# Optimization experiments

Hardware: AMD Instinct MI355X
Metric: run time of the kernel (lower is better)

The kernel has to match this reference:

```python
import jax, jax.numpy as jnp
import numpy as np

TOKENS, HIDDEN, N_EXPERTS = 16384, 2048, 64
JITTER_EPS = 0.01
Z_LOSS_COEFF = 0.001


def setup_inputs() -> dict:
    key = jax.random.key(0)
    k1, k2 = jax.random.split(key)
    x = jax.random.normal(k1, (TOKENS, HIDDEN), dtype=jnp.float32)
    w = jax.random.normal(k2, (N_EXPERTS, HIDDEN), dtype=jnp.float32) * 0.02  # router weight [E,H]
    return {"x": x, "w": w}


def _route_pass(scores_sel, scores, jitter_eps):
    # scores_sel: logits possibly with -inf at already-selected expert (top-2 pass)
    # scores:     original logits (used for abs/clamp factor, as in torch code)
    mx = jnp.max(scores_sel, axis=-1, keepdims=True)                      # [N,1]
    factor = jnp.maximum(jnp.abs(scores), mx)                             # scores.abs().clamp(min=mx)
    mask = jax.lax.stop_gradient((mx - scores) / factor > 2.0 * jitter_eps)
    masked_logits = jnp.where(mask, -jnp.inf, scores_sel)
    # eval path (training=False): selected_experts = argmax of (masked-for-selection) scores
    sel = jnp.argmax(scores_sel, axis=-1)[..., None]                      # [N,1] int
    gates = jax.nn.softmax(masked_logits, axis=-1)
    # mask_for_one: selected == argmax(gates) holds deterministically in eval -> 1.0
    mult = jnp.take_along_axis(gates, sel, axis=-1)                       # [N,1]
    return mult, sel


def reference(x, w):
    logits = x @ w.T                                                      # [N,E]
    # z-loss (identity on logits in forward; scalar returned for completeness)
    z_loss = Z_LOSS_COEFF * jnp.mean(jnp.square(jax.nn.logsumexp(logits, axis=-1)))
    original_gates = jax.nn.softmax(logits, axis=-1)
    # top-1 pass
    m1, s1 = _route_pass(logits, logits, JITTER_EPS)
    # top-2 pass: mask out the first selection
    e_idx = jnp.arange(logits.shape[-1])[None, :]
    scores2 = jnp.where(e_idx == s1, -jnp.inf, logits)
    m2, s2 = _route_pass(scores2, logits, JITTER_EPS)
    multiplier = jnp.concatenate([m1, m2], axis=-1)                       # [N,2]
    selected_experts = jnp.concatenate([s1, s2], axis=-1)                 # [N,2]
    return multiplier, original_gates, selected_experts, z_loss
```

## Files before the change

### kernel.cpp

```cpp
#include <hip/hip_runtime.h>
#include <math.h>

#define TOKENS 16384
#define HIDDEN 2048
#define NEXP   64
#define MT     16
#define NBLK   (TOKENS / MT)
#define BK     256
#define NCH    (HIDDEN / BK)
#define ROWB   1024

#define GATES_OFF (TOKENS * 2)
#define SEL_OFF   (GATES_OFF + TOKENS * NEXP)
#define Z_OFF     (SEL_OFF + TOKENS * 2)

#define WIMG_BYTES (NEXP * HIDDEN * 2 * 2)

typedef __attribute__((ext_vector_type(8))) _Float16 f16x8;
typedef __attribute__((ext_vector_type(4))) float    f32x4;

__device__ __forceinline__ float wave_sum64(float v) {
    #pragma unroll
    for (int s = 1; s < 64; s <<= 1) v += __shfl_xor(v, s, 64);
    return v;
}

__device__ __forceinline__ void dma16(const void* g, void* l) {
    __builtin_amdgcn_global_load_lds(
        (const __attribute__((address_space(1))) unsigned int*)g,
        (__attribute__((address_space(3))) unsigned int*)l, 16, 0, 0);
}

__global__ __launch_bounds__(256) void wconvert(
    const float* __restrict__ w, uint4* __restrict__ wimg)
{
    const int s = blockIdx.x * 256 + threadIdx.x;
    const int c    = s >> 10;
    const int r    = s & 1023;
    const int l    = r & 63;
    const int nt   = (r >> 6) & 1;
    const int kh   = (r >> 7) & 1;
    const int term = (r >> 8) & 1;
    const int eh   = (r >> 9) & 1;
    const int e = eh * 32 + nt * 16 + (l & 15);
    const int k = c * 64 + kh * 32 + (l >> 4) * 8;

    const float* src = w + (size_t)e * HIDDEN + k;
    union { _Float16 f[8]; uint4 u; } o;
    #pragma unroll
    for (int j = 0; j < 8; ++j) {
        const float v = src[j];
        const _Float16 h = (_Float16)v;
        o.f[j] = (term == 0) ? h : (_Float16)((v - (float)h) * 4096.f);
    }
    wimg[s] = o.u;
}

__device__ __forceinline__ void cvt_split(const float4 a, const float4 b,
                                          f16x8& hi, f16x8& lo) {
    union { _Float16 f[8]; f16x8 v; } H, L;
    #pragma unroll
    for (int j = 0; j < 4; ++j) {
        const float s0 = (&a.x)[j];
        const float s1 = (&b.x)[j];
        const _Float16 h0 = (_Float16)s0;
        const _Float16 h1 = (_Float16)s1;
        H.f[j]     = h0;
        H.f[j + 4] = h1;
        L.f[j]     = (_Float16)((s0 - (float)h0) * 4096.f);
        L.f[j + 4] = (_Float16)((s1 - (float)h1) * 4096.f);
    }
    hi = H.v; lo = L.v;
}

__global__ __launch_bounds__(256, 3) void router_main(
    const float* __restrict__ x, const uint4* __restrict__ wimg,
    float* __restrict__ out, float* __restrict__ zpartial)
{
    __shared__ __align__(16) unsigned char smem[2 * MT * ROWB];
    __shared__ float zred[4];
    float* lg = (float*)smem;

    const int tid  = threadIdx.x;
    const int wv   = __builtin_amdgcn_readfirstlane(tid >> 6);
    const int lane = tid & 63;
    const int t0   = blockIdx.x * MT;

    const int row_r = lane & 15;
    const int kgrp  = lane >> 4;
    const int sr    = (row_r & 7) << 4;

    const float* xg[4];
    #pragma unroll
    for (int p = 0; p < 4; ++p) {
        const int row  = wv * 4 + p;
        const int srow = (row & 7) << 4;
        xg[p] = x + (size_t)(t0 + row) * HIDDEN + (((lane * 16) ^ srow) >> 2);
    }

    f32x4 acc0[4], acc1[4];
    #pragma unroll
    for (int g = 0; g < 4; ++g) { acc0[g] = (f32x4)0.f; acc1[g] = (f32x4)0.f; }

    #pragma unroll
    for (int p = 0; p < 4; ++p)
        dma16(xg[p], smem + (wv * 4 + p) * ROWB);
    __syncthreads();

    #pragma unroll
    for (int c = 0; c < NCH; ++c) {
        const int buf = c & 1;

        const uint4* p0 = wimg + (size_t)(c * 4 + wv) * 1024 + lane;
        f16x8 bh[2][4], bl[2][4];
        #pragma unroll
        for (int st = 0; st < 2; ++st) {
            const uint4* p = p0 + st * 128;
            bh[st][0] = *(const f16x8*)(p);
            bh[st][1] = *(const f16x8*)(p + 64);
            bh[st][2] = *(const f16x8*)(p + 512);
            bh[st][3] = *(const f16x8*)(p + 576);
            bl[st][0] = *(const f16x8*)(p + 256);
            bl[st][1] = *(const f16x8*)(p + 320);
            bl[st][2] = *(const f16x8*)(p + 768);
            bl[st][3] = *(const f16x8*)(p + 832);
        }

        if (c + 1 < NCH) {
            #pragma unroll
            for (int p = 0; p < 4; ++p)
                dma16(xg[p] + (c + 1) * BK,
                      smem + (buf ^ 1) * (MT * ROWB) + (wv * 4 + p) * ROWB);
        }

        const unsigned char* abase = smem + buf * (MT * ROWB) + row_r * ROWB;
        #pragma unroll
        for (int st = 0; st < 2; ++st) {
            const int kb0 = wv * 256 + st * 128 + kgrp * 32;
            const float4 va = *(const float4*)(abase + (kb0 ^ sr));
            const float4 vb = *(const float4*)(abase + ((kb0 + 16) ^ sr));
            f16x8 Ah, Al;
            cvt_split(va, vb, Ah, Al);
            #pragma unroll
            for (int g = 0; g < 4; ++g) {
                acc0[g] = __builtin_amdgcn_mfma_f32_16x16x32_f16(Ah, bh[st][g], acc0[g], 0, 0, 0);
                acc1[g] = __builtin_amdgcn_mfma_f32_16x16x32_f16(Ah, bl[st][g], acc1[g], 0, 0, 0);
                acc1[g] = __builtin_amdgcn_mfma_f32_16x16x32_f16(Al, bh[st][g], acc1[g], 0, 0, 0);
            }
        }

        __syncthreads();
    }

    #pragma unroll
    for (int g = 0; g < 4; ++g)
        #pragma unroll
        for (int r = 0; r < 4; ++r) {
            const int tok = kgrp * 4 + r;
            const int e   = (g >> 1) * 32 + (g & 1) * 16 + row_r;
            lg[wv * (MT * 66) + tok * 66 + e] = acc0[g][r] + acc1[g][r] * (1.f / 4096.f);
        }
    __syncthreads();

    float zsum = 0.f;
    for (int tt = 0; tt < 4; ++tt) {
        const int t = wv * 4 + tt;
        const int li = t * 66 + lane;
        const float v = lg[0 * (MT * 66) + li] + lg[1 * (MT * 66) + li]
                      + lg[2 * (MT * 66) + li] + lg[3 * (MT * 66) + li];

        float bv = v; int bi = lane;
        #pragma unroll
        for (int s = 1; s < 64; s <<= 1) {
            const float ov = __shfl_xor(bv, s, 64);
            const int   oi = __shfl_xor(bi, s, 64);
            if (ov > bv || (ov == bv && oi < bi)) { bv = ov; bi = oi; }
        }
        const float max1 = bv; const int s1 = bi;

        const float e1 = expf(v - max1);
        const float sume = wave_sum64(e1);
        out[GATES_OFF + (size_t)(t0 + t) * NEXP + lane] = e1 / sume;
        const float lse = max1 + logf(sume);
        zsum += lse * lse;

        const bool mask1 = (max1 - v) > 0.02f * fmaxf(fabsf(v), max1);
        const float sum1 = wave_sum64(mask1 ? 0.f : e1);

        float bv2 = (lane == s1) ? -INFINITY : v; int bi2 = lane;
        #pragma unroll
        for (int s = 1; s < 64; s <<= 1) {
            const float ov = __shfl_xor(bv2, s, 64);
            const int   oi = __shfl_xor(bi2, s, 64);
            if (ov > bv2 || (ov == bv2 && oi < bi2)) { bv2 = ov; bi2 = oi; }
        }
        const float max2 = bv2; const int s2 = bi2;

        const bool mask2 = (max2 - v) > 0.02f * fmaxf(fabsf(v), max2);
        const float p2v = (mask2 || lane == s1) ? 0.f : expf(v - max2);
        const float sum2 = wave_sum64(p2v);

        if (lane == 0) {
            const size_t trow = (size_t)(t0 + t) * 2;
            out[trow + 0] = 1.f / sum1;
            out[trow + 1] = 1.f / sum2;
            out[SEL_OFF + trow + 0] = (float)s1;
            out[SEL_OFF + trow + 1] = (float)s2;
        }
    }

    if (lane == 0) zred[wv] = zsum;
    __syncthreads();
    if (tid == 0)
        zpartial[blockIdx.x] = zred[0] + zred[1] + zred[2] + zred[3];
}

__global__ __launch_bounds__(256) void zfinal(
    const float* __restrict__ zpartial, float* __restrict__ out)
{
    const int tid = threadIdx.x;
    float v = zpartial[tid] + zpartial[tid + 256]
            + zpartial[tid + 512] + zpartial[tid + 768];
    v = wave_sum64(v);
    __shared__ float red[4];
    if ((tid & 63) == 0) red[tid >> 6] = v;
    __syncthreads();
    if (tid == 0) {
        const float tot = red[0] + red[1] + red[2] + red[3];
        out[Z_OFF] = 0.001f * (tot / (float)TOKENS);
    }
}

extern "C" void kernel_launch(void* const* d_in, const int* in_sizes, int n_in,
                              void* d_out, int out_size, void* d_ws, size_t ws_size,
                              hipStream_t stream) {
    const float* x = (const float*)d_in[0];
    const float* w = (const float*)d_in[1];
    float* out = (float*)d_out;

    uint4* wimg     = (uint4*)d_ws;
    float* zpartial = (float*)((char*)d_ws + WIMG_BYTES);

    wconvert<<<128, 256, 0, stream>>>(w, wimg);
    router_main<<<NBLK, 256, 0, stream>>>(x, wimg, out, zpartial);
    zfinal<<<1, 256, 0, stream>>>(zpartial, out);
}
```

Measured before the change: 213.6 us.

## Use single-wave blocks covering full K, dropping cross-wave reduction and barriers

Each 16-token block now runs as one 64-lane wave that walks the whole hidden dimension instead of splitting K across four waves. This removes the LDS partial-logit reduction and all block barriers, and the routing softmax/top-2 epilogue works directly from the MFMA accumulators with 16-lane shuffles. The trade-off is four times as much serial MFMA and weight-load work per wave, with the x tile DMA double-buffered per wave and guarded only by vmcnt waits. Occupancy now relies on many small blocks instead of large ones.

```diff
diff --git a/kernel.cpp b/kernel.cpp
--- a/kernel.cpp
+++ b/kernel.cpp
@@ -8,7 +8,7 @@
 #define NBLK   (TOKENS / MT)
 #define BK     256
 #define NCH    (HIDDEN / BK)
-#define ROWB   1024
+#define CB     16384
 
 #define GATES_OFF (TOKENS * 2)
 #define SEL_OFF   (GATES_OFF + TOKENS * NEXP)
@@ -73,146 +73,146 @@
     hi = H.v; lo = L.v;
 }
 
-__global__ __launch_bounds__(256, 3) void router_main(
+__global__ __launch_bounds__(64) void router_main(
     const float* __restrict__ x, const uint4* __restrict__ wimg,
     float* __restrict__ out, float* __restrict__ zpartial)
 {
-    __shared__ __align__(16) unsigned char smem[2 * MT * ROWB];
-    __shared__ float zred[4];
-    float* lg = (float*)smem;
-
-    const int tid  = threadIdx.x;
-    const int wv   = __builtin_amdgcn_readfirstlane(tid >> 6);
-    const int lane = tid & 63;
+    __shared__ __align__(16) unsigned char smem[2 * CB];
+
+    const int lane = threadIdx.x & 63;
     const int t0   = blockIdx.x * MT;
-
-    const int row_r = lane & 15;
-    const int kgrp  = lane >> 4;
-    const int sr    = (row_r & 7) << 4;
-
-    const float* xg[4];
-    #pragma unroll
-    for (int p = 0; p < 4; ++p) {
-        const int row  = wv * 4 + p;
-        const int srow = (row & 7) << 4;
-        xg[p] = x + (size_t)(t0 + row) * HIDDEN + (((lane * 16) ^ srow) >> 2);
-    }
+    const int rowr = lane & 15;
+    const int kg   = lane >> 4;
+
+    const float* xq = x + (size_t)(t0 + rowr) * HIDDEN + kg * 4;
 
     f32x4 acc0[4], acc1[4];
     #pragma unroll
     for (int g = 0; g < 4; ++g) { acc0[g] = (f32x4)0.f; acc1[g] = (f32x4)0.f; }
 
     #pragma unroll
-    for (int p = 0; p < 4; ++p)
-        dma16(xg[p], smem + (wv * 4 + p) * ROWB);
-    __syncthreads();
-
-    #pragma unroll
+    for (int j = 0; j < 16; ++j)
+        dma16(xq + j * 16, smem + j * 1024);
+
     for (int c = 0; c < NCH; ++c) {
-        const int buf = c & 1;
-
-        const uint4* p0 = wimg + (size_t)(c * 4 + wv) * 1024 + lane;
-        f16x8 bh[2][4], bl[2][4];
-        #pragma unroll
-        for (int st = 0; st < 2; ++st) {
-            const uint4* p = p0 + st * 128;
-            bh[st][0] = *(const f16x8*)(p);
-            bh[st][1] = *(const f16x8*)(p + 64);
-            bh[st][2] = *(const f16x8*)(p + 512);
-            bh[st][3] = *(const f16x8*)(p + 576);
-            bl[st][0] = *(const f16x8*)(p + 256);
-            bl[st][1] = *(const f16x8*)(p + 320);
-            bl[st][2] = *(const f16x8*)(p + 768);
-            bl[st][3] = *(const f16x8*)(p + 832);
-        }
+        asm volatile("s_waitcnt vmcnt(0)" ::: "memory");
+        __builtin_amdgcn_sched_barrier(0);
 
         if (c + 1 < NCH) {
+            const float* sg = xq + (c + 1) * BK;
+            unsigned char* dg = smem + ((c + 1) & 1) * CB;
             #pragma unroll
-            for (int p = 0; p < 4; ++p)
-                dma16(xg[p] + (c + 1) * BK,
-                      smem + (buf ^ 1) * (MT * ROWB) + (wv * 4 + p) * ROWB);
-        }
-
-        const unsigned char* abase = smem + buf * (MT * ROWB) + row_r * ROWB;
-        #pragma unroll
-        for (int st = 0; st < 2; ++st) {
-            const int kb0 = wv * 256 + st * 128 + kgrp * 32;
-            const float4 va = *(const float4*)(abase + (kb0 ^ sr));
-            const float4 vb = *(const float4*)(abase + ((kb0 + 16) ^ sr));
+            for (int j = 0; j < 16; ++j)
+                dma16(sg + j * 16, dg + j * 1024);
+        }
+
+        const unsigned char* ab = smem + (c & 1) * CB + kg * 512 + rowr * 16;
+        const uint4* wc0 = wimg + (size_t)c * 4096 + lane;
+        #pragma unroll
+        for (int s = 0; s < 8; ++s) {
+            const uint4* p = wc0 + (s >> 1) * 1024 + (s & 1) * 128;
+            f16x8 bh[4], bl[4];
+            bh[0] = *(const f16x8*)(p);
+            bh[1] = *(const f16x8*)(p + 64);
+            bh[2] = *(const f16x8*)(p + 512);
+            bh[3] = *(const f16x8*)(p + 576);
+            bl[0] = *(const f16x8*)(p + 256);
+            bl[1] = *(const f16x8*)(p + 320);
+            bl[2] = *(const f16x8*)(p + 768);
+            bl[3] = *(const f16x8*)(p + 832);
+
+            const float4 va = *(const float4*)(ab + s * 2048);
+            const float4 vb = *(const float4*)(ab + s * 2048 + 256);
             f16x8 Ah, Al;
             cvt_split(va, vb, Ah, Al);
             #pragma unroll
             for (int g = 0; g < 4; ++g) {
-                acc0[g] = __builtin_amdgcn_mfma_f32_16x16x32_f16(Ah, bh[st][g], acc0[g], 0, 0, 0);
-                acc1[g] = __builtin_amdgcn_mfma_f32_16x16x32_f16(Ah, bl[st][g], acc1[g], 0, 0, 0);
-                acc1[g] = __builtin_amdgcn_mfma_f32_16x16x32_f16(Al, bh[st][g], acc1[g], 0, 0, 0);
+                acc0[g] = __builtin_amdgcn_mfma_f32_16x16x32_f16(Ah, bh[g], acc0[g], 0, 0, 0);
+                acc1[g] = __builtin_amdgcn_mfma_f32_16x16x32_f16(Ah, bl[g], acc1[g], 0, 0, 0);
+                acc1[g] = __builtin_amdgcn_mfma_f32_16x16x32_f16(Al, bh[g], acc1[g], 0, 0, 0);
             }
         }
-
-        __syncthreads();
-    }
-
-    #pragma unroll
-    for (int g = 0; g < 4; ++g)
-        #pragma unroll
-        for (int r = 0; r < 4; ++r) {
-            const int tok = kgrp * 4 + r;
-            const int e   = (g >> 1) * 32 + (g & 1) * 16 + row_r;
-            lg[wv * (MT * 66) + tok * 66 + e] = acc0[g][r] + acc1[g][r] * (1.f / 4096.f);
-        }
-    __syncthreads();
+    }
 
     float zsum = 0.f;
-    for (int tt = 0; tt < 4; ++tt) {
-        const int t = wv * 4 + tt;
-        const int li = t * 66 + lane;
-        const float v = lg[0 * (MT * 66) + li] + lg[1 * (MT * 66) + li]
-                      + lg[2 * (MT * 66) + li] + lg[3 * (MT * 66) + li];
-
-        float bv = v; int bi = lane;
-        #pragma unroll
-        for (int s = 1; s < 64; s <<= 1) {
-            const float ov = __shfl_xor(bv, s, 64);
-            const int   oi = __shfl_xor(bi, s, 64);
+    #pragma unroll
+    for (int r = 0; r < 4; ++r) {
+        const int t = kg * 4 + r;
+        float v[4]; int e[4];
+        #pragma unroll
+        for (int g = 0; g < 4; ++g) {
+            v[g] = acc0[g][r] + acc1[g][r] * (1.f / 4096.f);
+            e[g] = g * 16 + rowr;
+        }
+
+        float bv = v[0]; int bi = e[0];
+        #pragma unroll
+        for (int g = 1; g < 4; ++g)
+            if (v[g] > bv) { bv = v[g]; bi = e[g]; }
+        #pragma unroll
+        for (int st = 1; st < 16; st <<= 1) {
+            const float ov = __shfl_xor(bv, st, 64);
+            const int   oi = __shfl_xor(bi, st, 64);
             if (ov > bv || (ov == bv && oi < bi)) { bv = ov; bi = oi; }
         }
         const float max1 = bv; const int s1 = bi;
 
-        const float e1 = expf(v - max1);
-        const float sume = wave_sum64(e1);
-        out[GATES_OFF + (size_t)(t0 + t) * NEXP + lane] = e1 / sume;
-        const float lse = max1 + logf(sume);
-        zsum += lse * lse;
-
-        const bool mask1 = (max1 - v) > 0.02f * fmaxf(fabsf(v), max1);
-        const float sum1 = wave_sum64(mask1 ? 0.f : e1);
-
-        float bv2 = (lane == s1) ? -INFINITY : v; int bi2 = lane;
-        #pragma unroll
-        for (int s = 1; s < 64; s <<= 1) {
-            const float ov = __shfl_xor(bv2, s, 64);
-            const int   oi = __shfl_xor(bi2, s, 64);
+        float e1[4], se = 0.f, sm1 = 0.f;
+        #pragma unroll
+        for (int g = 0; g < 4; ++g) {
+            e1[g] = expf(v[g] - max1);
+            se += e1[g];
+            const bool m1 = (max1 - v[g]) > 0.02f * fmaxf(fabsf(v[g]), max1);
+            sm1 += m1 ? 0.f : e1[g];
+        }
+        #pragma unroll
+        for (int st = 1; st < 16; st <<= 1) {
+            se  += __shfl_xor(se, st, 64);
+            sm1 += __shfl_xor(sm1, st, 64);
+        }
+
+        #pragma unroll
+        for (int g = 0; g < 4; ++g)
+            out[GATES_OFF + (size_t)(t0 + t) * NEXP + e[g]] = e1[g] / se;
+
+        const float lse = max1 + logf(se);
+        if (rowr == 0) zsum += lse * lse;
+
+        float bv2 = (e[0] == s1) ? -INFINITY : v[0]; int bi2 = e[0];
+        #pragma unroll
+        for (int g = 1; g < 4; ++g) {
+            const float cv = (e[g] == s1) ? -INFINITY : v[g];
+            if (cv > bv2) { bv2 = cv; bi2 = e[g]; }
+        }
+        #pragma unroll
+        for (int st = 1; st < 16; st <<= 1) {
+            const float ov = __shfl_xor(bv2, st, 64);
+            const int   oi = __shfl_xor(bi2, st, 64);
             if (ov > bv2 || (ov == bv2 && oi < bi2)) { bv2 = ov; bi2 = oi; }
         }
         const float max2 = bv2; const int s2 = bi2;
 
-        const bool mask2 = (max2 - v) > 0.02f * fmaxf(fabsf(v), max2);
-        const float p2v = (mask2 || lane == s1) ? 0.f : expf(v - max2);
-        const float sum2 = wave_sum64(p2v);
-
-        if (lane == 0) {
+        float sm2 = 0.f;
+        #pragma unroll
+        for (int g = 0; g < 4; ++g) {
+            const bool m2 = (max2 - v[g]) > 0.02f * fmaxf(fabsf(v[g]), max2);
+            sm2 += (m2 || e[g] == s1) ? 0.f : expf(v[g] - max2);
+        }
+        #pragma unroll
+        for (int st = 1; st < 16; st <<= 1)
+            sm2 += __shfl_xor(sm2, st, 64);
+
+        if (rowr == 0) {
             const size_t trow = (size_t)(t0 + t) * 2;
-            out[trow + 0] = 1.f / sum1;
-            out[trow + 1] = 1.f / sum2;
+            out[trow + 0] = 1.f / sm1;
+            out[trow + 1] = 1.f / sm2;
             out[SEL_OFF + trow + 0] = (float)s1;
             out[SEL_OFF + trow + 1] = (float)s2;
         }
     }
 
-    if (lane == 0) zred[wv] = zsum;
-    __syncthreads();
-    if (tid == 0)
-        zpartial[blockIdx.x] = zred[0] + zred[1] + zred[2] + zred[3];
+    const float zt = wave_sum64(zsum);
+    if (lane == 0) zpartial[blockIdx.x] = zt;
 }
 
 __global__ __launch_bounds__(256) void zfinal(
@@ -242,6 +242,6 @@
     float* zpartial = (float*)((char*)d_ws + WIMG_BYTES);
 
     wconvert<<<128, 256, 0, stream>>>(w, wimg);
-    router_main<<<NBLK, 256, 0, stream>>>(x, wimg, out, zpartial);
+    router_main<<<NBLK, 64, 0, stream>>>(x, wimg, out, zpartial);
     zfinal<<<1, 256, 0, stream>>>(zpartial, out);
 }
```

New measurement: 236.2 us. 10.6% more time.
